# Optimization experiments

Measured on AMD Instinct MI355X. Metric: run time of the kernel, lower is better.

## Reference

```python
import jax, jax.numpy as jnp
import numpy as np

N = 100000      # nodes
E = 1600000     # edges (avg degree 16)
D_IN, D_H, D_OUT = 128, 128, 64


def setup_inputs() -> dict:
    key = jax.random.key(0)
    ks = jax.random.split(key, 9)
    x = jax.random.normal(ks[0], (N, D_IN), dtype=jnp.float32)
    edge_index = jax.random.randint(ks[1], (2, E), 0, N, dtype=jnp.int32)
    edge_weight = jax.random.uniform(ks[2], (E,), dtype=jnp.float32)
    def lin(k, fi, fo):
        return jax.random.normal(k, (fi, fo), dtype=jnp.float32) * np.float32(1.0 / np.sqrt(fi))
    w0 = lin(ks[3], D_IN, D_H);  b0 = jnp.zeros((D_H,), jnp.float32)
    w1 = lin(ks[4], D_H, D_H);   b1 = jnp.zeros((D_H,), jnp.float32)
    w2 = lin(ks[5], D_H, D_OUT); b2 = jnp.zeros((D_OUT,), jnp.float32)
    return {"x": x, "edge_index": edge_index, "edge_weight": edge_weight,
            "w0": w0, "b0": b0, "w1": w1, "b1": b1, "w2": w2, "b2": b2}


def _gcn_conv(x, row, col, norm, w, b):
    # x: [N, fi] -> [N, fo].  PyG GCNConv: linear, gather src, scale, scatter to dst, + bias
    h = x @ w                                   # [N, fo]
    msg = h[row] * norm[:, None]                # [E+N, fo] gather + scale
    out = jax.ops.segment_sum(msg, col, num_segments=N)  # scatter-add to dst
    return out + b


def reference(x, edge_index, edge_weight, w0, b0, w1, b1, w2, b2):
    # add self-loops with weight 1 (PyG gcn_norm default)
    loops = jnp.arange(N, dtype=edge_index.dtype)
    row = jnp.concatenate([edge_index[0], loops])
    col = jnp.concatenate([edge_index[1], loops])
    ew = jnp.concatenate([edge_weight, jnp.ones((N,), edge_weight.dtype)])
    deg = jax.ops.segment_sum(ew, col, num_segments=N)          # in-degree by weight
    dis = jnp.where(deg > 0, jax.lax.rsqrt(deg), 0.0)
    norm = dis[row] * dis[col] * ew                             # [E+N]

    h = _gcn_conv(x, row, col, norm, w0, b0)
    h = jax.nn.relu(h)                                          # dropout: eval mode (identity)
    h = _gcn_conv(h, row, col, norm, w1, b1)
    h = jax.nn.relu(h)
    out = _gcn_conv(h, row, col, norm, w2, b2)
    return out
```

## Files before the change

### kernel.cpp

```cpp
#include <hip/hip_runtime.h>
#include <hip/hip_fp16.h>

typedef __attribute__((ext_vector_type(8))) short bf16x8;
typedef __attribute__((ext_vector_type(4))) float f32x4;

#define EW_SCALE (1.0f / 32767.0f)
#define NBMAX 1024
#define BCAP  4096
#define CHUNK 3072

__device__ __forceinline__ unsigned bf16_rne(float v) {
  unsigned u = __float_as_uint(v);
  return (u + 0x7FFFu + ((u >> 16) & 1u)) >> 16;
}

__global__ __launch_bounds__(256) void bin_fill(const int* __restrict__ row,
    const int* __restrict__ col, const float* __restrict__ ew,
    int* __restrict__ gcnt, uint2* __restrict__ binned, int E) {
  __shared__ uint2 stage[CHUNK];
  __shared__ int cnt_s[NBMAX];
  __shared__ int off_s[NBMAX];
  __shared__ int cur_s[NBMAX];
  __shared__ int gb_s[NBMAX];
  __shared__ int partial[256];
  const int t = threadIdx.x;
  const int base = blockIdx.x * CHUNK;
  const int n = min(CHUNK, E - base);
  for (int k = t; k < NBMAX; k += 256) cnt_s[k] = 0;
  __syncthreads();
  for (int k = t; k < n; k += 256) atomicAdd(&cnt_s[((unsigned)col[base + k]) >> 7], 1);
  __syncthreads();
  int loc[4]; int s0 = 0;
#pragma unroll
  for (int j = 0; j < 4; ++j) { loc[j] = cnt_s[t * 4 + j]; s0 += loc[j]; }
  partial[t] = s0;
  __syncthreads();
  for (int o = 1; o < 256; o <<= 1) {
    int x = (t >= o) ? partial[t - o] : 0;
    __syncthreads();
    partial[t] += x;
    __syncthreads();
  }
  int run = partial[t] - s0;
#pragma unroll
  for (int j = 0; j < 4; ++j) { off_s[t * 4 + j] = run; cur_s[t * 4 + j] = run; run += loc[j]; }
  __syncthreads();
  for (int b = t; b < NBMAX; b += 256) {
    int c = cnt_s[b];
    if (c > 0) gb_s[b] = atomicAdd(&gcnt[b], c);
  }
  for (int k = t; k < n; k += 256) {
    int e = base + k;
    int s = row[e];
    unsigned d = (unsigned)col[e];
    int q = (int)(ew[e] * 32767.0f + 0.5f); if (q > 32767) q = 32767;
    uint2 r = make_uint2(((unsigned)s << 15) | (unsigned)q, d);
    int p = atomicAdd(&cur_s[d >> 7], 1);
    stage[p] = r;
  }
  __syncthreads();
  for (int k = t; k < n; k += 256) {
    uint2 r = stage[k];
    int b = r.y >> 7;
    int pos = gb_s[b] + (k - off_s[b]);
    if (pos < BCAP) binned[(long)b * BCAP + pos] = r;
  }
}

__global__ __launch_bounds__(256) void bucket_build(const uint2* __restrict__ binned,
    const int* __restrict__ gcnt, unsigned* __restrict__ slots,
    int* __restrict__ pdeg, float* __restrict__ dis, int N) {
  __shared__ int cur[128];
  __shared__ float acc[128];
  const int b = blockIdx.x, t = threadIdx.x;
  const int node0 = b << 7;
  int cnt = gcnt[b]; if (cnt > BCAP) cnt = BCAP;
  if (t < 128) { cur[t] = 0; acc[t] = 0.f; }
  __syncthreads();
  for (int k = t; k < cnt; k += 256) {
    uint2 r = binned[(long)b * BCAP + k];
    int nl = r.y & 127;
    int p = atomicAdd(&cur[nl], 1);
    if (p < 64) {
      slots[(long)(node0 + nl) * 64 + p] = r.x;
      atomicAdd(&acc[nl], (float)(r.x & 0x7FFFu) * EW_SCALE);
    }
  }
  __syncthreads();
  if (t < 128) {
    int node = node0 + t;
    if (node < N) {
      int deg = cur[t]; if (deg > 64) deg = 64;
      int pad = (deg + 7) & ~7;
      for (int j = deg; j < pad; ++j) slots[(long)node * 64 + j] = 0u;
      pdeg[node] = pad;
      dis[node] = rsqrtf(1.0f + acc[t]);
    }
  }
}

template<int FO>
__device__ __forceinline__ void prep_w_dev(const float* __restrict__ w,
    ushort* __restrict__ wp, int idx) {
  constexpr int GROUPS = (FO / 16) * 4 * 64;
  constexpr int PLANE  = GROUPS * 8;
  if (idx >= GROUPS) return;
  int l = idx & 63;
  int ts = idx >> 6;
  int s = ts & 3, t = ts >> 2;
  unsigned hi[8], lo[8];
#pragma unroll
  for (int j = 0; j < 8; ++j) {
    float v = w[(s * 32 + (l >> 4) * 8 + j) * FO + t * 16 + (l & 15)];
    unsigned r = bf16_rne(v);
    hi[j] = r;
    float res = v - __uint_as_float(r << 16);
    lo[j] = bf16_rne(res);
  }
  uint4 ph, pl;
  ph.x = hi[0] | (hi[1] << 16); ph.y = hi[2] | (hi[3] << 16);
  ph.z = hi[4] | (hi[5] << 16); ph.w = hi[6] | (hi[7] << 16);
  pl.x = lo[0] | (lo[1] << 16); pl.y = lo[2] | (lo[3] << 16);
  pl.z = lo[4] | (lo[5] << 16); pl.w = lo[6] | (lo[7] << 16);
  *reinterpret_cast<uint4*>(&wp[idx * 8])         = ph;
  *reinterpret_cast<uint4*>(&wp[PLANE + idx * 8]) = pl;
}

__global__ __launch_bounds__(256) void prep_all(const float* __restrict__ w0,
    const float* __restrict__ w1, const float* __restrict__ w2,
    ushort* __restrict__ wp0, ushort* __restrict__ wp1, ushort* __restrict__ wp2,
    int* __restrict__ gcnt) {
  const int b = blockIdx.x, t = threadIdx.x;
  if (b < 8)       prep_w_dev<128>(w0, wp0, b * 256 + t);
  else if (b < 16) prep_w_dev<128>(w1, wp1, (b - 8) * 256 + t);
  else if (b < 20) prep_w_dev<64>(w2, wp2, (b - 16) * 256 + t);
  else { int k = (b - 20) * 256 + t; if (k < NBMAX) gcnt[k] = 0; }
}

template<int FO, bool HIN>
__global__ __launch_bounds__(256) void gemm_mfma(const void* __restrict__ inv,
    const ushort* __restrict__ wp, const float* __restrict__ dis,
    __half* __restrict__ out, int M) {
  constexpr int NT = FO / 16;
  constexpr int PLANE = NT * 4 * 64 * 8;
  __shared__ __attribute__((aligned(16))) ushort sW[2 * PLANE];
  const int tid = threadIdx.x;
  for (int i = tid; i < PLANE / 4; i += 256)
    reinterpret_cast<uint4*>(sW)[i] = reinterpret_cast<const uint4*>(wp)[i];
  __syncthreads();

  const int wave = tid >> 6, lane = tid & 63;
  const int rowA = blockIdx.x * 64 + wave * 16 + (lane & 15);
  const int kblk = lane >> 4;
  const bool rowok = rowA < M;

  f32x4 acc[NT];
#pragma unroll
  for (int t = 0; t < NT; ++t) acc[t] = (f32x4){0.f, 0.f, 0.f, 0.f};

#pragma unroll
  for (int s = 0; s < 4; ++s) {
    float v[8];
    if (rowok) {
      if constexpr (HIN) {
        const __half* inH = (const __half*)inv;
        __half hv[8];
        *reinterpret_cast<uint4*>(hv) =
            *reinterpret_cast<const uint4*>(&inH[(long)rowA * 128 + s * 32 + kblk * 8]);
#pragma unroll
        for (int j = 0; j < 8; ++j) v[j] = __half2float(hv[j]);
      } else {
        const float* inF = (const float*)inv;
        float4 p0 = *reinterpret_cast<const float4*>(&inF[(long)rowA * 128 + s * 32 + kblk * 8]);
        float4 p1 = *reinterpret_cast<const float4*>(&inF[(long)rowA * 128 + s * 32 + kblk * 8 + 4]);
        v[0] = p0.x; v[1] = p0.y; v[2] = p0.z; v[3] = p0.w;
        v[4] = p1.x; v[5] = p1.y; v[6] = p1.z; v[7] = p1.w;
      }
    } else {
#pragma unroll
      for (int j = 0; j < 8; ++j) v[j] = 0.f;
    }
    bf16x8 ah, al;
#pragma unroll
    for (int j = 0; j < 8; ++j) {
      unsigned r = bf16_rne(v[j]);
      ah[j] = (short)(ushort)r;
      float res = v[j] - __uint_as_float(r << 16);
      al[j] = (short)(ushort)bf16_rne(res);
    }
#pragma unroll
    for (int t = 0; t < NT; ++t) {
      bf16x8 bh = *reinterpret_cast<const bf16x8*>(&sW[((t * 4 + s) * 64 + lane) * 8]);
      bf16x8 bl = *reinterpret_cast<const bf16x8*>(&sW[PLANE + ((t * 4 + s) * 64 + lane) * 8]);
      acc[t] = __builtin_amdgcn_mfma_f32_16x16x32_bf16(ah, bh, acc[t], 0, 0, 0);
      acc[t] = __builtin_amdgcn_mfma_f32_16x16x32_bf16(ah, bl, acc[t], 0, 0, 0);
      acc[t] = __builtin_amdgcn_mfma_f32_16x16x32_bf16(al, bh, acc[t], 0, 0, 0);
    }
  }

  const int rbase = blockIdx.x * 64 + wave * 16 + (lane >> 4) * 4;
#pragma unroll
  for (int r = 0; r < 4; ++r) {
    int rr = rbase + r;
    if (rr < M) {
      float ds = dis[rr];
#pragma unroll
      for (int t = 0; t < NT; ++t)
        out[(long)rr * FO + t * 16 + (lane & 15)] = __float2half_rn(ds * acc[t][r]);
    }
  }
}

template<bool RELU>
__global__ __launch_bounds__(256) void agg128_kernel(const __half* __restrict__ g,
    const int* __restrict__ pdeg, const unsigned* __restrict__ slots,
    const float* __restrict__ dis, const float* __restrict__ bias,
    __half* __restrict__ out, int N) {
  const int wave = threadIdx.x >> 6, lane = threadIdx.x & 63;
  const int i = blockIdx.x * 4 + wave;
  if (i >= N) return;
  const int iu = __builtin_amdgcn_readfirstlane(i);
  const __half2* __restrict__ gp = reinterpret_cast<const __half2*>(g);
  const float d = dis[iu];
  const float2 gv = __half22float2(gp[(long)iu * 64 + lane]);
  const int dp = pdeg[iu];
  const unsigned* __restrict__ sp = slots + ((long)iu << 6);
  float accx = 0.f, accy = 0.f;
  for (int j = 0; j < dp; j += 8) {
    uint4 a = *reinterpret_cast<const uint4*>(sp + j);
    uint4 b = *reinterpret_cast<const uint4*>(sp + j + 4);
    __half2 h0 = gp[((long)(a.x >> 15) << 6) + lane];
    __half2 h1 = gp[((long)(a.y >> 15) << 6) + lane];
    __half2 h2 = gp[((long)(a.z >> 15) << 6) + lane];
    __half2 h3 = gp[((long)(a.w >> 15) << 6) + lane];
    __half2 h4 = gp[((long)(b.x >> 15) << 6) + lane];
    __half2 h5 = gp[((long)(b.y >> 15) << 6) + lane];
    __half2 h6 = gp[((long)(b.z >> 15) << 6) + lane];
    __half2 h7 = gp[((long)(b.w >> 15) << 6) + lane];
    float w0 = (float)(a.x & 0x7FFFu), w1 = (float)(a.y & 0x7FFFu);
    float w2 = (float)(a.z & 0x7FFFu), w3 = (float)(a.w & 0x7FFFu);
    float w4 = (float)(b.x & 0x7FFFu), w5 = (float)(b.y & 0x7FFFu);
    float w6 = (float)(b.z & 0x7FFFu), w7 = (float)(b.w & 0x7FFFu);
    accx = fmaf(w0, __low2float(h0), accx); accy = fmaf(w0, __high2float(h0), accy);
    accx = fmaf(w1, __low2float(h1), accx); accy = fmaf(w1, __high2float(h1), accy);
    accx = fmaf(w2, __low2float(h2), accx); accy = fmaf(w2, __high2float(h2), accy);
    accx = fmaf(w3, __low2float(h3), accx); accy = fmaf(w3, __high2float(h3), accy);
    accx = fmaf(w4, __low2float(h4), accx); accy = fmaf(w4, __high2float(h4), accy);
    accx = fmaf(w5, __low2float(h5), accx); accy = fmaf(w5, __high2float(h5), accy);
    accx = fmaf(w6, __low2float(h6), accx); accy = fmaf(w6, __high2float(h6), accy);
    accx = fmaf(w7, __low2float(h7), accx); accy = fmaf(w7, __high2float(h7), accy);
  }
  const float2 bv = reinterpret_cast<const float2*>(bias)[lane];
  float vx = fmaf(d, fmaf(EW_SCALE, accx, gv.x), bv.x);
  float vy = fmaf(d, fmaf(EW_SCALE, accy, gv.y), bv.y);
  if (RELU) { vx = fmaxf(vx, 0.f); vy = fmaxf(vy, 0.f); }
  reinterpret_cast<__half2*>(out)[(long)i * 64 + lane] = __floats2half2_rn(vx, vy);
}

template<bool RELU>
__global__ __launch_bounds__(256) void agg64_kernel(const __half* __restrict__ g,
    const int* __restrict__ pdeg, const unsigned* __restrict__ slots,
    const float* __restrict__ dis, const float* __restrict__ bias,
    float* __restrict__ out, int N) {
  const int wave = threadIdx.x >> 6, lane = threadIdx.x & 63;
  const int i = blockIdx.x * 4 + wave;
  if (i >= N) return;
  const int iu = __builtin_amdgcn_readfirstlane(i);
  const float d = dis[iu];
  const float gv = __half2float(g[(long)iu * 64 + lane]);
  const int dp = pdeg[iu];
  const unsigned* __restrict__ sp = slots + ((long)iu << 6);
  float acc = 0.f;
  for (int j = 0; j < dp; j += 8) {
    uint4 a = *reinterpret_cast<const uint4*>(sp + j);
    uint4 b = *reinterpret_cast<const uint4*>(sp + j + 4);
    __half h0 = g[((long)(a.x >> 15) << 6) + lane];
    __half h1 = g[((long)(a.y >> 15) << 6) + lane];
    __half h2 = g[((long)(a.z >> 15) << 6) + lane];
    __half h3 = g[((long)(a.w >> 15) << 6) + lane];
    __half h4 = g[((long)(b.x >> 15) << 6) + lane];
    __half h5 = g[((long)(b.y >> 15) << 6) + lane];
    __half h6 = g[((long)(b.z >> 15) << 6) + lane];
    __half h7 = g[((long)(b.w >> 15) << 6) + lane];
    acc = fmaf((float)(a.x & 0x7FFFu), __half2float(h0), acc);
    acc = fmaf((float)(a.y & 0x7FFFu), __half2float(h1), acc);
    acc = fmaf((float)(a.z & 0x7FFFu), __half2float(h2), acc);
    acc = fmaf((float)(a.w & 0x7FFFu), __half2float(h3), acc);
    acc = fmaf((float)(b.x & 0x7FFFu), __half2float(h4), acc);
    acc = fmaf((float)(b.y & 0x7FFFu), __half2float(h5), acc);
    acc = fmaf((float)(b.z & 0x7FFFu), __half2float(h6), acc);
    acc = fmaf((float)(b.w & 0x7FFFu), __half2float(h7), acc);
  }
  float v = fmaf(d, fmaf(EW_SCALE, acc, gv), bias[lane]);
  if (RELU) v = fmaxf(v, 0.f);
  out[(long)i * 64 + lane] = v;
}

extern "C" void kernel_launch(void* const* d_in, const int* in_sizes, int n_in,
                              void* d_out, int out_size, void* d_ws, size_t ws_size,
                              hipStream_t stream) {
  const float* x  = (const float*)d_in[0];
  const int*   ei = (const int*)  d_in[1];
  const float* ew = (const float*)d_in[2];
  const float* w0 = (const float*)d_in[3];
  const float* b0 = (const float*)d_in[4];
  const float* w1 = (const float*)d_in[5];
  const float* b1 = (const float*)d_in[6];
  const float* w2 = (const float*)d_in[7];
  const float* b2 = (const float*)d_in[8];

  const int N = in_sizes[0] / 128;
  const int E = in_sizes[2];
  const int* row = ei;
  const int* col = ei + E;
  const int NB = (N + 127) / 128;

  auto align16 = [](size_t v) { return (v + 15) & ~(size_t)15; };
  const long NF = (long)N * 128;

  size_t off = 0;
  __half*   bufA   = (__half*)((char*)d_ws + off); off = align16(off + NF * sizeof(__half));
  __half*   bufB   = (__half*)((char*)d_ws + off); off = align16(off + NF * sizeof(__half));
  unsigned* slots  = (unsigned*)((char*)d_ws + off); off = align16(off + (size_t)N * 64 * 4);
  uint2*    binned = (uint2*)((char*)d_ws + off); off = align16(off + (size_t)NB * BCAP * 8);
  int*      gcnt   = (int*)((char*)d_ws + off); off = align16(off + (size_t)NBMAX * 4);
  int*      pdeg   = (int*)((char*)d_ws + off); off = align16(off + (size_t)N * 4);
  float*    dis    = (float*)((char*)d_ws + off); off = align16(off + (size_t)N * 4);
  const size_t WP128 = 2ull * 8 * 4 * 64 * 8 * sizeof(ushort);
  ushort*   wp0    = (ushort*)((char*)d_ws + off); off += WP128;
  ushort*   wp1    = (ushort*)((char*)d_ws + off); off += WP128;
  ushort*   wp2    = (ushort*)((char*)d_ws + off); off += WP128 / 2;
  if (ws_size < off) return;

  auto cdiv = [](long a, long b) { return (int)((a + b - 1) / b); };

  prep_all<<<24, 256, 0, stream>>>(w0, w1, w2, wp0, wp1, wp2, gcnt);

  bin_fill    <<<cdiv(E,CHUNK),256,0,stream>>>(row, col, ew, gcnt, binned, E);
  bucket_build<<<NB,256,0,stream>>>(binned, gcnt, slots, pdeg, dis, N);

  gemm_mfma<128,false><<<cdiv(N,64),256,0,stream>>>(x, wp0, dis, bufA, N);
  agg128_kernel<true><<<cdiv(N,4),256,0,stream>>>(bufA, pdeg, slots, dis, b0, bufB, N);
  gemm_mfma<128,true><<<cdiv(N,64),256,0,stream>>>(bufB, wp1, dis, bufA, N);
  agg128_kernel<true><<<cdiv(N,4),256,0,stream>>>(bufA, pdeg, slots, dis, b1, bufB, N);
  gemm_mfma<64,true><<<cdiv(N,64),256,0,stream>>>(bufB, wp2, dis, bufA, N);
  agg64_kernel<false><<<cdiv(N,4),256,0,stream>>>(bufA, pdeg, slots, dis, b2, (float*)d_out, N);
}
```

Measured before the change: 277.9 us.

## Fuse aggregation with next-layer GEMM via LDS-staged bf16 split tiles

Merges each 128-wide aggregation (bias, ReLU) with the following layer's MFMA GEMM. Each block aggregates 64 nodes into XOR-swizzled LDS as hi/lo bf16 pairs, then multiplies them by the weights, which are read straight from global memory. This removes the fp16 round trip of the intermediate activations and two launches. The first GEMM now processes 128 rows per block so its weight staging is amortised. The risk is lower occupancy, since each wave serially gathers 16 nodes before the MFMA phase, with no overlap between gather and compute.

```diff
diff --git a/kernel.cpp b/kernel.cpp
--- a/kernel.cpp
+++ b/kernel.cpp
@@ -137,11 +137,10 @@
   else { int k = (b - 20) * 256 + t; if (k < NBMAX) gcnt[k] = 0; }
 }
 
-template<int FO, bool HIN>
-__global__ __launch_bounds__(256) void gemm_mfma(const void* __restrict__ inv,
+__global__ __launch_bounds__(256) void gemm0(const float* __restrict__ in,
     const ushort* __restrict__ wp, const float* __restrict__ dis,
     __half* __restrict__ out, int M) {
-  constexpr int NT = FO / 16;
+  constexpr int NT = 8;
   constexpr int PLANE = NT * 4 * 64 * 8;
   __shared__ __attribute__((aligned(16))) ushort sW[2 * PLANE];
   const int tid = threadIdx.x;
@@ -150,114 +149,153 @@
   __syncthreads();
 
   const int wave = tid >> 6, lane = tid & 63;
-  const int rowA = blockIdx.x * 64 + wave * 16 + (lane & 15);
   const int kblk = lane >> 4;
-  const bool rowok = rowA < M;
-
-  f32x4 acc[NT];
-#pragma unroll
-  for (int t = 0; t < NT; ++t) acc[t] = (f32x4){0.f, 0.f, 0.f, 0.f};
-
-#pragma unroll
-  for (int s = 0; s < 4; ++s) {
-    float v[8];
-    if (rowok) {
-      if constexpr (HIN) {
-        const __half* inH = (const __half*)inv;
-        __half hv[8];
-        *reinterpret_cast<uint4*>(hv) =
-            *reinterpret_cast<const uint4*>(&inH[(long)rowA * 128 + s * 32 + kblk * 8]);
-#pragma unroll
-        for (int j = 0; j < 8; ++j) v[j] = __half2float(hv[j]);
-      } else {
-        const float* inF = (const float*)inv;
-        float4 p0 = *reinterpret_cast<const float4*>(&inF[(long)rowA * 128 + s * 32 + kblk * 8]);
-        float4 p1 = *reinterpret_cast<const float4*>(&inF[(long)rowA * 128 + s * 32 + kblk * 8 + 4]);
+
+  for (int half = 0; half < 2; ++half) {
+    const int rowA = blockIdx.x * 128 + half * 64 + wave * 16 + (lane & 15);
+    const bool rowok = rowA < M;
+    f32x4 acc[NT];
+#pragma unroll
+    for (int t = 0; t < NT; ++t) acc[t] = (f32x4){0.f, 0.f, 0.f, 0.f};
+#pragma unroll
+    for (int s = 0; s < 4; ++s) {
+      float v[8];
+      if (rowok) {
+        float4 p0 = *reinterpret_cast<const float4*>(&in[(long)rowA * 128 + s * 32 + kblk * 8]);
+        float4 p1 = *reinterpret_cast<const float4*>(&in[(long)rowA * 128 + s * 32 + kblk * 8 + 4]);
         v[0] = p0.x; v[1] = p0.y; v[2] = p0.z; v[3] = p0.w;
         v[4] = p1.x; v[5] = p1.y; v[6] = p1.z; v[7] = p1.w;
-      }
-    } else {
-#pragma unroll
-      for (int j = 0; j < 8; ++j) v[j] = 0.f;
-    }
-    bf16x8 ah, al;
-#pragma unroll
-    for (int j = 0; j < 8; ++j) {
-      unsigned r = bf16_rne(v[j]);
-      ah[j] = (short)(ushort)r;
-      float res = v[j] - __uint_as_float(r << 16);
-      al[j] = (short)(ushort)bf16_rne(res);
-    }
+      } else {
+#pragma unroll
+        for (int j = 0; j < 8; ++j) v[j] = 0.f;
+      }
+      bf16x8 ah, al;
+#pragma unroll
+      for (int j = 0; j < 8; ++j) {
+        unsigned r = bf16_rne(v[j]);
+        ah[j] = (short)(ushort)r;
+        float res = v[j] - __uint_as_float(r << 16);
+        al[j] = (short)(ushort)bf16_rne(res);
+      }
+#pragma unroll
+      for (int t = 0; t < NT; ++t) {
+        bf16x8 bh = *reinterpret_cast<const bf16x8*>(&sW[((t * 4 + s) * 64 + lane) * 8]);
+        bf16x8 bl = *reinterpret_cast<const bf16x8*>(&sW[PLANE + ((t * 4 + s) * 64 + lane) * 8]);
+        acc[t] = __builtin_amdgcn_mfma_f32_16x16x32_bf16(ah, bh, acc[t], 0, 0, 0);
+        acc[t] = __builtin_amdgcn_mfma_f32_16x16x32_bf16(ah, bl, acc[t], 0, 0, 0);
+        acc[t] = __builtin_amdgcn_mfma_f32_16x16x32_bf16(al, bh, acc[t], 0, 0, 0);
+      }
+    }
+    const int rbase = blockIdx.x * 128 + half * 64 + wave * 16 + (lane >> 4) * 4;
+#pragma unroll
+    for (int r = 0; r < 4; ++r) {
+      int rr = rbase + r;
+      if (rr < M) {
+        float ds = dis[rr];
+#pragma unroll
+        for (int t = 0; t < NT; ++t)
+          out[(long)rr * 128 + t * 16 + (lane & 15)] = __float2half_rn(ds * acc[t][r]);
+      }
+    }
+  }
+}
+
+template<int FO>
+__global__ __launch_bounds__(256) void fused_agg_gemm(const __half* __restrict__ g,
+    const int* __restrict__ pdeg, const unsigned* __restrict__ slots,
+    const float* __restrict__ dis, const float* __restrict__ bias,
+    const ushort* __restrict__ wp, __half* __restrict__ out, int N) {
+  constexpr int NT = FO / 16;
+  constexpr int PLANE = NT * 4 * 64 * 8;
+  __shared__ __attribute__((aligned(16))) unsigned tHi[64 * 64];
+  __shared__ __attribute__((aligned(16))) unsigned tLo[64 * 64];
+  const int tid = threadIdx.x;
+  const int w = tid >> 6, lane = tid & 63;
+  const int base = blockIdx.x * 64;
+  const __half2* __restrict__ gp = reinterpret_cast<const __half2*>(g);
+  const float2 bv = reinterpret_cast<const float2*>(bias)[lane];
+
+  for (int k = 0; k < 16; ++k) {
+    const int r = w * 16 + k;
+    const int node = __builtin_amdgcn_readfirstlane(base + r);
+    float vx = 0.f, vy = 0.f;
+    if (node < N) {
+      const float d = dis[node];
+      const float2 gv = __half22float2(gp[(long)node * 64 + lane]);
+      const int dp = pdeg[node];
+      const unsigned* __restrict__ sp = slots + ((long)node << 6);
+      float accx = 0.f, accy = 0.f;
+      for (int j = 0; j < dp; j += 8) {
+        uint4 a = *reinterpret_cast<const uint4*>(sp + j);
+        uint4 b = *reinterpret_cast<const uint4*>(sp + j + 4);
+        __half2 h0 = gp[((long)(a.x >> 15) << 6) + lane];
+        __half2 h1 = gp[((long)(a.y >> 15) << 6) + lane];
+        __half2 h2 = gp[((long)(a.z >> 15) << 6) + lane];
+        __half2 h3 = gp[((long)(a.w >> 15) << 6) + lane];
+        __half2 h4 = gp[((long)(b.x >> 15) << 6) + lane];
+        __half2 h5 = gp[((long)(b.y >> 15) << 6) + lane];
+        __half2 h6 = gp[((long)(b.z >> 15) << 6) + lane];
+        __half2 h7 = gp[((long)(b.w >> 15) << 6) + lane];
+        float w0 = (float)(a.x & 0x7FFFu), w1 = (float)(a.y & 0x7FFFu);
+        float w2 = (float)(a.z & 0x7FFFu), w3 = (float)(a.w & 0x7FFFu);
+        float w4 = (float)(b.x & 0x7FFFu), w5 = (float)(b.y & 0x7FFFu);
+        float w6 = (float)(b.z & 0x7FFFu), w7 = (float)(b.w & 0x7FFFu);
+        accx = fmaf(w0, __low2float(h0), accx); accy = fmaf(w0, __high2float(h0), accy);
+        accx = fmaf(w1, __low2float(h1), accx); accy = fmaf(w1, __high2float(h1), accy);
+        accx = fmaf(w2, __low2float(h2), accx); accy = fmaf(w2, __high2float(h2), accy);
+        accx = fmaf(w3, __low2float(h3), accx); accy = fmaf(w3, __high2float(h3), accy);
+        accx = fmaf(w4, __low2float(h4), accx); accy = fmaf(w4, __high2float(h4), accy);
+        accx = fmaf(w5, __low2float(h5), accx); accy = fmaf(w5, __high2float(h5), accy);
+        accx = fmaf(w6, __low2float(h6), accx); accy = fmaf(w6, __high2float(h6), accy);
+        accx = fmaf(w7, __low2float(h7), accx); accy = fmaf(w7, __high2float(h7), accy);
+      }
+      vx = fmaxf(fmaf(d, fmaf(EW_SCALE, accx, gv.x), bv.x), 0.f);
+      vy = fmaxf(fmaf(d, fmaf(EW_SCALE, accy, gv.y), bv.y), 0.f);
+    }
+    unsigned hx = bf16_rne(vx), hy = bf16_rne(vy);
+    float rx = vx - __uint_as_float(hx << 16);
+    float ry = vy - __uint_as_float(hy << 16);
+    unsigned lx = bf16_rne(rx), ly = bf16_rne(ry);
+    const int phys = (lane >> 2) ^ k;
+    const int idx = r * 64 + phys * 4 + (lane & 3);
+    tHi[idx] = hx | (hy << 16);
+    tLo[idx] = lx | (ly << 16);
+  }
+  __syncthreads();
+
+  const int r15 = lane & 15, kblk = lane >> 4;
+  f32x4 acc[NT];
+#pragma unroll
+  for (int t = 0; t < NT; ++t) acc[t] = (f32x4){0.f, 0.f, 0.f, 0.f};
+#pragma unroll
+  for (int s = 0; s < 4; ++s) {
+    const int slot = s * 4 + kblk;
+    const int phys = slot ^ r15;
+    const int idx = (w * 16 + r15) * 64 + phys * 4;
+    bf16x8 ah = *reinterpret_cast<const bf16x8*>(&tHi[idx]);
+    bf16x8 al = *reinterpret_cast<const bf16x8*>(&tLo[idx]);
 #pragma unroll
     for (int t = 0; t < NT; ++t) {
-      bf16x8 bh = *reinterpret_cast<const bf16x8*>(&sW[((t * 4 + s) * 64 + lane) * 8]);
-      bf16x8 bl = *reinterpret_cast<const bf16x8*>(&sW[PLANE + ((t * 4 + s) * 64 + lane) * 8]);
+      bf16x8 bh = *reinterpret_cast<const bf16x8*>(&wp[((t * 4 + s) * 64 + lane) * 8]);
+      bf16x8 bl = *reinterpret_cast<const bf16x8*>(&wp[PLANE + ((t * 4 + s) * 64 + lane) * 8]);
       acc[t] = __builtin_amdgcn_mfma_f32_16x16x32_bf16(ah, bh, acc[t], 0, 0, 0);
       acc[t] = __builtin_amdgcn_mfma_f32_16x16x32_bf16(ah, bl, acc[t], 0, 0, 0);
       acc[t] = __builtin_amdgcn_mfma_f32_16x16x32_bf16(al, bh, acc[t], 0, 0, 0);
     }
   }
-
-  const int rbase = blockIdx.x * 64 + wave * 16 + (lane >> 4) * 4;
+  const int rbase = base + w * 16 + (lane >> 4) * 4;
 #pragma unroll
   for (int r = 0; r < 4; ++r) {
     int rr = rbase + r;
-    if (rr < M) {
+    if (rr < N) {
       float ds = dis[rr];
 #pragma unroll
       for (int t = 0; t < NT; ++t)
-        out[(long)rr * FO + t * 16 + (lane & 15)] = __float2half_rn(ds * acc[t][r]);
-    }
-  }
-}
-
-template<bool RELU>
-__global__ __launch_bounds__(256) void agg128_kernel(const __half* __restrict__ g,
-    const int* __restrict__ pdeg, const unsigned* __restrict__ slots,
-    const float* __restrict__ dis, const float* __restrict__ bias,
-    __half* __restrict__ out, int N) {
-  const int wave = threadIdx.x >> 6, lane = threadIdx.x & 63;
-  const int i = blockIdx.x * 4 + wave;
-  if (i >= N) return;
-  const int iu = __builtin_amdgcn_readfirstlane(i);
-  const __half2* __restrict__ gp = reinterpret_cast<const __half2*>(g);
-  const float d = dis[iu];
-  const float2 gv = __half22float2(gp[(long)iu * 64 + lane]);
-  const int dp = pdeg[iu];
-  const unsigned* __restrict__ sp = slots + ((long)iu << 6);
-  float accx = 0.f, accy = 0.f;
-  for (int j = 0; j < dp; j += 8) {
-    uint4 a = *reinterpret_cast<const uint4*>(sp + j);
-    uint4 b = *reinterpret_cast<const uint4*>(sp + j + 4);
-    __half2 h0 = gp[((long)(a.x >> 15) << 6) + lane];
-    __half2 h1 = gp[((long)(a.y >> 15) << 6) + lane];
-    __half2 h2 = gp[((long)(a.z >> 15) << 6) + lane];
-    __half2 h3 = gp[((long)(a.w >> 15) << 6) + lane];
-    __half2 h4 = gp[((long)(b.x >> 15) << 6) + lane];
-    __half2 h5 = gp[((long)(b.y >> 15) << 6) + lane];
-    __half2 h6 = gp[((long)(b.z >> 15) << 6) + lane];
-    __half2 h7 = gp[((long)(b.w >> 15) << 6) + lane];
-    float w0 = (float)(a.x & 0x7FFFu), w1 = (float)(a.y & 0x7FFFu);
-    float w2 = (float)(a.z & 0x7FFFu), w3 = (float)(a.w & 0x7FFFu);
-    float w4 = (float)(b.x & 0x7FFFu), w5 = (float)(b.y & 0x7FFFu);
-    float w6 = (float)(b.z & 0x7FFFu), w7 = (float)(b.w & 0x7FFFu);
-    accx = fmaf(w0, __low2float(h0), accx); accy = fmaf(w0, __high2float(h0), accy);
-    accx = fmaf(w1, __low2float(h1), accx); accy = fmaf(w1, __high2float(h1), accy);
-    accx = fmaf(w2, __low2float(h2), accx); accy = fmaf(w2, __high2float(h2), accy);
-    accx = fmaf(w3, __low2float(h3), accx); accy = fmaf(w3, __high2float(h3), accy);
-    accx = fmaf(w4, __low2float(h4), accx); accy = fmaf(w4, __high2float(h4), accy);
-    accx = fmaf(w5, __low2float(h5), accx); accy = fmaf(w5, __high2float(h5), accy);
-    accx = fmaf(w6, __low2float(h6), accx); accy = fmaf(w6, __high2float(h6), accy);
-    accx = fmaf(w7, __low2float(h7), accx); accy = fmaf(w7, __high2float(h7), accy);
-  }
-  const float2 bv = reinterpret_cast<const float2*>(bias)[lane];
-  float vx = fmaf(d, fmaf(EW_SCALE, accx, gv.x), bv.x);
-  float vy = fmaf(d, fmaf(EW_SCALE, accy, gv.y), bv.y);
-  if (RELU) { vx = fmaxf(vx, 0.f); vy = fmaxf(vy, 0.f); }
-  reinterpret_cast<__half2*>(out)[(long)i * 64 + lane] = __floats2half2_rn(vx, vy);
-}
-
-template<bool RELU>
+        out[(long)rr * FO + t * 16 + r15] = __float2half_rn(ds * acc[t][r]);
+    }
+  }
+}
+
 __global__ __launch_bounds__(256) void agg64_kernel(const __half* __restrict__ g,
     const int* __restrict__ pdeg, const unsigned* __restrict__ slots,
     const float* __restrict__ dis, const float* __restrict__ bias,
@@ -292,7 +330,6 @@
     acc = fmaf((float)(b.w & 0x7FFFu), __half2float(h7), acc);
   }
   float v = fmaf(d, fmaf(EW_SCALE, acc, gv), bias[lane]);
-  if (RELU) v = fmaxf(v, 0.f);
   out[(long)i * 64 + lane] = v;
 }
 
@@ -339,10 +376,8 @@
   bin_fill    <<<cdiv(E,CHUNK),256,0,stream>>>(row, col, ew, gcnt, binned, E);
   bucket_build<<<NB,256,0,stream>>>(binned, gcnt, slots, pdeg, dis, N);
 
-  gemm_mfma<128,false><<<cdiv(N,64),256,0,stream>>>(x, wp0, dis, bufA, N);
-  agg128_kernel<true><<<cdiv(N,4),256,0,stream>>>(bufA, pdeg, slots, dis, b0, bufB, N);
-  gemm_mfma<128,true><<<cdiv(N,64),256,0,stream>>>(bufB, wp1, dis, bufA, N);
-  agg128_kernel<true><<<cdiv(N,4),256,0,stream>>>(bufA, pdeg, slots, dis, b1, bufB, N);
-  gemm_mfma<64,true><<<cdiv(N,64),256,0,stream>>>(bufB, wp2, dis, bufA, N);
-  agg64_kernel<false><<<cdiv(N,4),256,0,stream>>>(bufA, pdeg, slots, dis, b2, (float*)d_out, N);
-}
+  gemm0<<<cdiv(N,128),256,0,stream>>>(x, wp0, dis, bufA, N);
+  fused_agg_gemm<128><<<cdiv(N,64),256,0,stream>>>(bufA, pdeg, slots, dis, b0, wp1, bufB, N);
+  fused_agg_gemm<64><<<cdiv(N,64),256,0,stream>>>(bufB, pdeg, slots, dis, b1, wp2, bufA, N);
+  agg64_kernel<<<cdiv(N,4),256,0,stream>>>(bufA, pdeg, slots, dis, b2, (float*)d_out, N);
+}
```

New measurement: 279.6 us. Within noise of the previous version (+0.6%).

## Fuse edge binning with first GEMM and move source normalization into aggregation

Applied to the files above, without the earlier changes.

The first-layer GEMM no longer depends on the degree normalization, because the source-side dis scaling now happens inside the aggregation kernels as a per-edge dis[src] gather. That lets the binning, the layer-0 GEMM with in-block weight prep, and the w1/w2 prep run in one combined launch instead of several serial ones. The GEMMs now handle 128 rows per block, and the gcnt reset becomes a memset. The cost is an extra random dis gather per edge in every aggregation pass, plus a combined kernel whose 64KB shared allocation applies to every block.

```diff
diff --git a/kernel.cpp b/kernel.cpp
--- a/kernel.cpp
+++ b/kernel.cpp
@@ -12,91 +12,6 @@
 __device__ __forceinline__ unsigned bf16_rne(float v) {
   unsigned u = __float_as_uint(v);
   return (u + 0x7FFFu + ((u >> 16) & 1u)) >> 16;
-}
-
-__global__ __launch_bounds__(256) void bin_fill(const int* __restrict__ row,
-    const int* __restrict__ col, const float* __restrict__ ew,
-    int* __restrict__ gcnt, uint2* __restrict__ binned, int E) {
-  __shared__ uint2 stage[CHUNK];
-  __shared__ int cnt_s[NBMAX];
-  __shared__ int off_s[NBMAX];
-  __shared__ int cur_s[NBMAX];
-  __shared__ int gb_s[NBMAX];
-  __shared__ int partial[256];
-  const int t = threadIdx.x;
-  const int base = blockIdx.x * CHUNK;
-  const int n = min(CHUNK, E - base);
-  for (int k = t; k < NBMAX; k += 256) cnt_s[k] = 0;
-  __syncthreads();
-  for (int k = t; k < n; k += 256) atomicAdd(&cnt_s[((unsigned)col[base + k]) >> 7], 1);
-  __syncthreads();
-  int loc[4]; int s0 = 0;
-#pragma unroll
-  for (int j = 0; j < 4; ++j) { loc[j] = cnt_s[t * 4 + j]; s0 += loc[j]; }
-  partial[t] = s0;
-  __syncthreads();
-  for (int o = 1; o < 256; o <<= 1) {
-    int x = (t >= o) ? partial[t - o] : 0;
-    __syncthreads();
-    partial[t] += x;
-    __syncthreads();
-  }
-  int run = partial[t] - s0;
-#pragma unroll
-  for (int j = 0; j < 4; ++j) { off_s[t * 4 + j] = run; cur_s[t * 4 + j] = run; run += loc[j]; }
-  __syncthreads();
-  for (int b = t; b < NBMAX; b += 256) {
-    int c = cnt_s[b];
-    if (c > 0) gb_s[b] = atomicAdd(&gcnt[b], c);
-  }
-  for (int k = t; k < n; k += 256) {
-    int e = base + k;
-    int s = row[e];
-    unsigned d = (unsigned)col[e];
-    int q = (int)(ew[e] * 32767.0f + 0.5f); if (q > 32767) q = 32767;
-    uint2 r = make_uint2(((unsigned)s << 15) | (unsigned)q, d);
-    int p = atomicAdd(&cur_s[d >> 7], 1);
-    stage[p] = r;
-  }
-  __syncthreads();
-  for (int k = t; k < n; k += 256) {
-    uint2 r = stage[k];
-    int b = r.y >> 7;
-    int pos = gb_s[b] + (k - off_s[b]);
-    if (pos < BCAP) binned[(long)b * BCAP + pos] = r;
-  }
-}
-
-__global__ __launch_bounds__(256) void bucket_build(const uint2* __restrict__ binned,
-    const int* __restrict__ gcnt, unsigned* __restrict__ slots,
-    int* __restrict__ pdeg, float* __restrict__ dis, int N) {
-  __shared__ int cur[128];
-  __shared__ float acc[128];
-  const int b = blockIdx.x, t = threadIdx.x;
-  const int node0 = b << 7;
-  int cnt = gcnt[b]; if (cnt > BCAP) cnt = BCAP;
-  if (t < 128) { cur[t] = 0; acc[t] = 0.f; }
-  __syncthreads();
-  for (int k = t; k < cnt; k += 256) {
-    uint2 r = binned[(long)b * BCAP + k];
-    int nl = r.y & 127;
-    int p = atomicAdd(&cur[nl], 1);
-    if (p < 64) {
-      slots[(long)(node0 + nl) * 64 + p] = r.x;
-      atomicAdd(&acc[nl], (float)(r.x & 0x7FFFu) * EW_SCALE);
-    }
-  }
-  __syncthreads();
-  if (t < 128) {
-    int node = node0 + t;
-    if (node < N) {
-      int deg = cur[t]; if (deg > 64) deg = 64;
-      int pad = (deg + 7) & ~7;
-      for (int j = deg; j < pad; ++j) slots[(long)node * 64 + j] = 0u;
-      pdeg[node] = pad;
-      dis[node] = rsqrtf(1.0f + acc[t]);
-    }
-  }
 }
 
 template<int FO>
@@ -126,21 +41,183 @@
   *reinterpret_cast<uint4*>(&wp[PLANE + idx * 8]) = pl;
 }
 
-__global__ __launch_bounds__(256) void prep_all(const float* __restrict__ w0,
-    const float* __restrict__ w1, const float* __restrict__ w2,
-    ushort* __restrict__ wp0, ushort* __restrict__ wp1, ushort* __restrict__ wp2,
-    int* __restrict__ gcnt) {
+__device__ void bin_fill_dev(const int* __restrict__ row, const int* __restrict__ col,
+    const float* __restrict__ ew, int* __restrict__ gcnt, uint2* __restrict__ binned,
+    int E, int blk, int t, char* smem) {
+  uint2* stage = (uint2*)smem;
+  int* cnt_s = (int*)(smem + 24576);
+  int* off_s = cnt_s + NBMAX;
+  int* cur_s = off_s + NBMAX;
+  int* gb_s  = cur_s + NBMAX;
+  int* partial = gb_s + NBMAX;
+  const int base = blk * CHUNK;
+  const int n = min(CHUNK, E - base);
+  for (int k = t; k < NBMAX; k += 256) cnt_s[k] = 0;
+  __syncthreads();
+  for (int k = t; k < n; k += 256) atomicAdd(&cnt_s[((unsigned)col[base + k]) >> 7], 1);
+  __syncthreads();
+  int loc[4]; int s0 = 0;
+#pragma unroll
+  for (int j = 0; j < 4; ++j) { loc[j] = cnt_s[t * 4 + j]; s0 += loc[j]; }
+  partial[t] = s0;
+  __syncthreads();
+  for (int o = 1; o < 256; o <<= 1) {
+    int x = (t >= o) ? partial[t - o] : 0;
+    __syncthreads();
+    partial[t] += x;
+    __syncthreads();
+  }
+  int run = partial[t] - s0;
+#pragma unroll
+  for (int j = 0; j < 4; ++j) { off_s[t * 4 + j] = run; cur_s[t * 4 + j] = run; run += loc[j]; }
+  __syncthreads();
+  for (int b = t; b < NBMAX; b += 256) {
+    int c = cnt_s[b];
+    if (c > 0) gb_s[b] = atomicAdd(&gcnt[b], c);
+  }
+  for (int k = t; k < n; k += 256) {
+    int e = base + k;
+    int s = row[e];
+    unsigned d = (unsigned)col[e];
+    int q = (int)(ew[e] * 32767.0f + 0.5f); if (q > 32767) q = 32767;
+    uint2 r = make_uint2(((unsigned)s << 15) | (unsigned)q, d);
+    int p = atomicAdd(&cur_s[d >> 7], 1);
+    stage[p] = r;
+  }
+  __syncthreads();
+  for (int k = t; k < n; k += 256) {
+    uint2 r = stage[k];
+    int b = r.y >> 7;
+    int pos = gb_s[b] + (k - off_s[b]);
+    if (pos < BCAP) binned[(long)b * BCAP + pos] = r;
+  }
+}
+
+__device__ void gemm0_dev(const float* __restrict__ in, const float* __restrict__ w0,
+    __half* __restrict__ out, int M, int blk, int tid, ushort* sW) {
+  constexpr int NT = 8;
+  constexpr int PLANE = NT * 4 * 64 * 8;
+  for (int idx = tid; idx < NT * 4 * 64; idx += 256) {
+    int l = idx & 63, ts = idx >> 6, s = ts & 3, tt = ts >> 2;
+    unsigned hi[8], lo[8];
+#pragma unroll
+    for (int j = 0; j < 8; ++j) {
+      float v = w0[(s * 32 + (l >> 4) * 8 + j) * 128 + tt * 16 + (l & 15)];
+      unsigned r = bf16_rne(v);
+      hi[j] = r;
+      float res = v - __uint_as_float(r << 16);
+      lo[j] = bf16_rne(res);
+    }
+    uint4 ph, pl;
+    ph.x = hi[0] | (hi[1] << 16); ph.y = hi[2] | (hi[3] << 16);
+    ph.z = hi[4] | (hi[5] << 16); ph.w = hi[6] | (hi[7] << 16);
+    pl.x = lo[0] | (lo[1] << 16); pl.y = lo[2] | (lo[3] << 16);
+    pl.z = lo[4] | (lo[5] << 16); pl.w = lo[6] | (lo[7] << 16);
+    *reinterpret_cast<uint4*>(&sW[idx * 8])         = ph;
+    *reinterpret_cast<uint4*>(&sW[PLANE + idx * 8]) = pl;
+  }
+  __syncthreads();
+
+  const int wave = tid >> 6, lane = tid & 63;
+  const int kblk = lane >> 4, r15 = lane & 15;
+  for (int half = 0; half < 2; ++half) {
+    const int rowA = blk * 128 + half * 64 + wave * 16 + r15;
+    const bool rowok = rowA < M;
+    f32x4 acc[NT];
+#pragma unroll
+    for (int t = 0; t < NT; ++t) acc[t] = (f32x4){0.f, 0.f, 0.f, 0.f};
+#pragma unroll
+    for (int s = 0; s < 4; ++s) {
+      float v[8];
+      if (rowok) {
+        float4 p0 = *reinterpret_cast<const float4*>(&in[(long)rowA * 128 + s * 32 + kblk * 8]);
+        float4 p1 = *reinterpret_cast<const float4*>(&in[(long)rowA * 128 + s * 32 + kblk * 8 + 4]);
+        v[0] = p0.x; v[1] = p0.y; v[2] = p0.z; v[3] = p0.w;
+        v[4] = p1.x; v[5] = p1.y; v[6] = p1.z; v[7] = p1.w;
+      } else {
+#pragma unroll
+        for (int j = 0; j < 8; ++j) v[j] = 0.f;
+      }
+      bf16x8 ah, al;
+#pragma unroll
+      for (int j = 0; j < 8; ++j) {
+        unsigned r = bf16_rne(v[j]);
+        ah[j] = (short)(ushort)r;
+        float res = v[j] - __uint_as_float(r << 16);
+        al[j] = (short)(ushort)bf16_rne(res);
+      }
+#pragma unroll
+      for (int t = 0; t < NT; ++t) {
+        bf16x8 bh = *reinterpret_cast<const bf16x8*>(&sW[((t * 4 + s) * 64 + lane) * 8]);
+        bf16x8 bl = *reinterpret_cast<const bf16x8*>(&sW[PLANE + ((t * 4 + s) * 64 + lane) * 8]);
+        acc[t] = __builtin_amdgcn_mfma_f32_16x16x32_bf16(ah, bh, acc[t], 0, 0, 0);
+        acc[t] = __builtin_amdgcn_mfma_f32_16x16x32_bf16(ah, bl, acc[t], 0, 0, 0);
+        acc[t] = __builtin_amdgcn_mfma_f32_16x16x32_bf16(al, bh, acc[t], 0, 0, 0);
+      }
+    }
+    const int rbase = blk * 128 + half * 64 + wave * 16 + (lane >> 4) * 4;
+#pragma unroll
+    for (int r = 0; r < 4; ++r) {
+      int rr = rbase + r;
+      if (rr < M) {
+#pragma unroll
+        for (int t = 0; t < NT; ++t)
+          out[(long)rr * 128 + t * 16 + r15] = __float2half_rn(acc[t][r]);
+      }
+    }
+  }
+}
+
+__global__ __launch_bounds__(256) void combo0(const float* __restrict__ x,
+    const float* __restrict__ w0, const float* __restrict__ w1, const float* __restrict__ w2,
+    ushort* __restrict__ wp1, ushort* __restrict__ wp2,
+    const int* __restrict__ row, const int* __restrict__ col, const float* __restrict__ ew,
+    int* __restrict__ gcnt, uint2* __restrict__ binned, __half* __restrict__ bufA,
+    int N, int E, int NBF, int G0) {
+  __shared__ __attribute__((aligned(16))) char smem[65536];
+  const int b = blockIdx.x, tid = threadIdx.x;
+  if (b < NBF) { bin_fill_dev(row, col, ew, gcnt, binned, E, b, tid, smem); return; }
+  if (b < NBF + G0) { gemm0_dev(x, w0, bufA, N, b - NBF, tid, (ushort*)smem); return; }
+  int pb = b - NBF - G0;
+  if (pb < 8) prep_w_dev<128>(w1, wp1, pb * 256 + tid);
+  else        prep_w_dev<64>(w2, wp2, (pb - 8) * 256 + tid);
+}
+
+__global__ __launch_bounds__(256) void bucket_build(const uint2* __restrict__ binned,
+    const int* __restrict__ gcnt, unsigned* __restrict__ slots,
+    int* __restrict__ pdeg, float* __restrict__ dis, int N) {
+  __shared__ int cur[128];
+  __shared__ float acc[128];
   const int b = blockIdx.x, t = threadIdx.x;
-  if (b < 8)       prep_w_dev<128>(w0, wp0, b * 256 + t);
-  else if (b < 16) prep_w_dev<128>(w1, wp1, (b - 8) * 256 + t);
-  else if (b < 20) prep_w_dev<64>(w2, wp2, (b - 16) * 256 + t);
-  else { int k = (b - 20) * 256 + t; if (k < NBMAX) gcnt[k] = 0; }
-}
-
-template<int FO, bool HIN>
-__global__ __launch_bounds__(256) void gemm_mfma(const void* __restrict__ inv,
-    const ushort* __restrict__ wp, const float* __restrict__ dis,
-    __half* __restrict__ out, int M) {
+  const int node0 = b << 7;
+  int cnt = gcnt[b]; if (cnt > BCAP) cnt = BCAP;
+  if (t < 128) { cur[t] = 0; acc[t] = 0.f; }
+  __syncthreads();
+  for (int k = t; k < cnt; k += 256) {
+    uint2 r = binned[(long)b * BCAP + k];
+    int nl = r.y & 127;
+    int p = atomicAdd(&cur[nl], 1);
+    if (p < 64) {
+      slots[(long)(node0 + nl) * 64 + p] = r.x;
+      atomicAdd(&acc[nl], (float)(r.x & 0x7FFFu) * EW_SCALE);
+    }
+  }
+  __syncthreads();
+  if (t < 128) {
+    int node = node0 + t;
+    if (node < N) {
+      int deg = cur[t]; if (deg > 64) deg = 64;
+      int pad = (deg + 7) & ~7;
+      for (int j = deg; j < pad; ++j) slots[(long)node * 64 + j] = 0u;
+      pdeg[node] = pad;
+      dis[node] = rsqrtf(1.0f + acc[t]);
+    }
+  }
+}
+
+template<int FO>
+__global__ __launch_bounds__(256) void gemm_mfma(const __half* __restrict__ in,
+    const ushort* __restrict__ wp, __half* __restrict__ out, int M) {
   constexpr int NT = FO / 16;
   constexpr int PLANE = NT * 4 * 64 * 8;
   __shared__ __attribute__((aligned(16))) ushort sW[2 * PLANE];
@@ -150,63 +227,52 @@
   __syncthreads();
 
   const int wave = tid >> 6, lane = tid & 63;
-  const int rowA = blockIdx.x * 64 + wave * 16 + (lane & 15);
-  const int kblk = lane >> 4;
-  const bool rowok = rowA < M;
-
-  f32x4 acc[NT];
-#pragma unroll
-  for (int t = 0; t < NT; ++t) acc[t] = (f32x4){0.f, 0.f, 0.f, 0.f};
-
-#pragma unroll
-  for (int s = 0; s < 4; ++s) {
-    float v[8];
-    if (rowok) {
-      if constexpr (HIN) {
-        const __half* inH = (const __half*)inv;
+  const int kblk = lane >> 4, r15 = lane & 15;
+  for (int half = 0; half < 2; ++half) {
+    const int rowA = blockIdx.x * 128 + half * 64 + wave * 16 + r15;
+    const bool rowok = rowA < M;
+    f32x4 acc[NT];
+#pragma unroll
+    for (int t = 0; t < NT; ++t) acc[t] = (f32x4){0.f, 0.f, 0.f, 0.f};
+#pragma unroll
+    for (int s = 0; s < 4; ++s) {
+      float v[8];
+      if (rowok) {
         __half hv[8];
         *reinterpret_cast<uint4*>(hv) =
-            *reinterpret_cast<const uint4*>(&inH[(long)rowA * 128 + s * 32 + kblk * 8]);
+            *reinterpret_cast<const uint4*>(&in[(long)rowA * 128 + s * 32 + kblk * 8]);
 #pragma unroll
         for (int j = 0; j < 8; ++j) v[j] = __half2float(hv[j]);
       } else {
-        const float* inF = (const float*)inv;
-        float4 p0 = *reinterpret_cast<const float4*>(&inF[(long)rowA * 128 + s * 32 + kblk * 8]);
-        float4 p1 = *reinterpret_cast<const float4*>(&inF[(long)rowA * 128 + s * 32 + kblk * 8 + 4]);
-        v[0] = p0.x; v[1] = p0.y; v[2] = p0.z; v[3] = p0.w;
-        v[4] = p1.x; v[5] = p1.y; v[6] = p1.z; v[7] = p1.w;
-      }
-    } else {
-#pragma unroll
-      for (int j = 0; j < 8; ++j) v[j] = 0.f;
-    }
-    bf16x8 ah, al;
-#pragma unroll
-    for (int j = 0; j < 8; ++j) {
-      unsigned r = bf16_rne(v[j]);
-      ah[j] = (short)(ushort)r;
-      float res = v[j] - __uint_as_float(r << 16);
-      al[j] = (short)(ushort)bf16_rne(res);
-    }
-#pragma unroll
-    for (int t = 0; t < NT; ++t) {
-      bf16x8 bh = *reinterpret_cast<const bf16x8*>(&sW[((t * 4 + s) * 64 + lane) * 8]);
-      bf16x8 bl = *reinterpret_cast<const bf16x8*>(&sW[PLANE + ((t * 4 + s) * 64 + lane) * 8]);
-      acc[t] = __builtin_amdgcn_mfma_f32_16x16x32_bf16(ah, bh, acc[t], 0, 0, 0);
-      acc[t] = __builtin_amdgcn_mfma_f32_16x16x32_bf16(ah, bl, acc[t], 0, 0, 0);
-      acc[t] = __builtin_amdgcn_mfma_f32_16x16x32_bf16(al, bh, acc[t], 0, 0, 0);
-    }
-  }
-
-  const int rbase = blockIdx.x * 64 + wave * 16 + (lane >> 4) * 4;
-#pragma unroll
-  for (int r = 0; r < 4; ++r) {
-    int rr = rbase + r;
-    if (rr < M) {
-      float ds = dis[rr];
-#pragma unroll
-      for (int t = 0; t < NT; ++t)
-        out[(long)rr * FO + t * 16 + (lane & 15)] = __float2half_rn(ds * acc[t][r]);
+#pragma unroll
+        for (int j = 0; j < 8; ++j) v[j] = 0.f;
+      }
+      bf16x8 ah, al;
+#pragma unroll
+      for (int j = 0; j < 8; ++j) {
+        unsigned r = bf16_rne(v[j]);
+        ah[j] = (short)(ushort)r;
+        float res = v[j] - __uint_as_float(r << 16);
+        al[j] = (short)(ushort)bf16_rne(res);
+      }
+#pragma unroll
+      for (int t = 0; t < NT; ++t) {
+        bf16x8 bh = *reinterpret_cast<const bf16x8*>(&sW[((t * 4 + s) * 64 + lane) * 8]);
+        bf16x8 bl = *reinterpret_cast<const bf16x8*>(&sW[PLANE + ((t * 4 + s) * 64 + lane) * 8]);
+        acc[t] = __builtin_amdgcn_mfma_f32_16x16x32_bf16(ah, bh, acc[t], 0, 0, 0);
+        acc[t] = __builtin_amdgcn_mfma_f32_16x16x32_bf16(ah, bl, acc[t], 0, 0, 0);
+        acc[t] = __builtin_amdgcn_mfma_f32_16x16x32_bf16(al, bh, acc[t], 0, 0, 0);
+      }
+    }
+    const int rbase = blockIdx.x * 128 + half * 64 + wave * 16 + (lane >> 4) * 4;
+#pragma unroll
+    for (int r = 0; r < 4; ++r) {
+      int rr = rbase + r;
+      if (rr < M) {
+#pragma unroll
+        for (int t = 0; t < NT; ++t)
+          out[(long)rr * FO + t * 16 + r15] = __float2half_rn(acc[t][r]);
+      }
     }
   }
 }
@@ -221,7 +287,7 @@
   if (i >= N) return;
   const int iu = __builtin_amdgcn_readfirstlane(i);
   const __half2* __restrict__ gp = reinterpret_cast<const __half2*>(g);
-  const float d = dis[iu];
+  const float dd = dis[iu];
   const float2 gv = __half22float2(gp[(long)iu * 64 + lane]);
   const int dp = pdeg[iu];
   const unsigned* __restrict__ sp = slots + ((long)iu << 6);
@@ -237,10 +303,14 @@
     __half2 h5 = gp[((long)(b.y >> 15) << 6) + lane];
     __half2 h6 = gp[((long)(b.z >> 15) << 6) + lane];
     __half2 h7 = gp[((long)(b.w >> 15) << 6) + lane];
-    float w0 = (float)(a.x & 0x7FFFu), w1 = (float)(a.y & 0x7FFFu);
-    float w2 = (float)(a.z & 0x7FFFu), w3 = (float)(a.w & 0x7FFFu);
-    float w4 = (float)(b.x & 0x7FFFu), w5 = (float)(b.y & 0x7FFFu);
-    float w6 = (float)(b.z & 0x7FFFu), w7 = (float)(b.w & 0x7FFFu);
+    float w0 = (float)(a.x & 0x7FFFu) * dis[a.x >> 15];
+    float w1 = (float)(a.y & 0x7FFFu) * dis[a.y >> 15];
+    float w2 = (float)(a.z & 0x7FFFu) * dis[a.z >> 15];
+    float w3 = (float)(a.w & 0x7FFFu) * dis[a.w >> 15];
+    float w4 = (float)(b.x & 0x7FFFu) * dis[b.x >> 15];
+    float w5 = (float)(b.y & 0x7FFFu) * dis[b.y >> 15];
+    float w6 = (float)(b.z & 0x7FFFu) * dis[b.z >> 15];
+    float w7 = (float)(b.w & 0x7FFFu) * dis[b.w >> 15];
     accx = fmaf(w0, __low2float(h0), accx); accy = fmaf(w0, __high2float(h0), accy);
     accx = fmaf(w1, __low2float(h1), accx); accy = fmaf(w1, __high2float(h1), accy);
     accx = fmaf(w2, __low2float(h2), accx); accy = fmaf(w2, __high2float(h2), accy);
@@ -251,13 +321,13 @@
     accx = fmaf(w7, __low2float(h7), accx); accy = fmaf(w7, __high2float(h7), accy);
   }
   const float2 bv = reinterpret_cast<const float2*>(bias)[lane];
-  float vx = fmaf(d, fmaf(EW_SCALE, accx, gv.x), bv.x);
-  float vy = fmaf(d, fmaf(EW_SCALE, accy, gv.y), bv.y);
+  const float dds = dd * EW_SCALE, dd2 = dd * dd;
+  float vx = fmaf(dds, accx, fmaf(dd2, gv.x, bv.x));
+  float vy = fmaf(dds, accy, fmaf(dd2, gv.y, bv.y));
   if (RELU) { vx = fmaxf(vx, 0.f); vy = fmaxf(vy, 0.f); }
   reinterpret_cast<__half2*>(out)[(long)i * 64 + lane] = __floats2half2_rn(vx, vy);
 }
 
-template<bool RELU>
 __global__ __launch_bounds__(256) void agg64_kernel(const __half* __restrict__ g,
     const int* __restrict__ pdeg, const unsigned* __restrict__ slots,
     const float* __restrict__ dis, const float* __restrict__ bias,
@@ -266,7 +336,7 @@
   const int i = blockIdx.x * 4 + wave;
   if (i >= N) return;
   const int iu = __builtin_amdgcn_readfirstlane(i);
-  const float d = dis[iu];
+  const float dd = dis[iu];
   const float gv = __half2float(g[(long)iu * 64 + lane]);
   const int dp = pdeg[iu];
   const unsigned* __restrict__ sp = slots + ((long)iu << 6);
@@ -282,18 +352,25 @@
     __half h5 = g[((long)(b.y >> 15) << 6) + lane];
     __half h6 = g[((long)(b.z >> 15) << 6) + lane];
     __half h7 = g[((long)(b.w >> 15) << 6) + lane];
-    acc = fmaf((float)(a.x & 0x7FFFu), __half2float(h0), acc);
-    acc = fmaf((float)(a.y & 0x7FFFu), __half2float(h1), acc);
-    acc = fmaf((float)(a.z & 0x7FFFu), __half2float(h2), acc);
-    acc = fmaf((float)(a.w & 0x7FFFu), __half2float(h3), acc);
-    acc = fmaf((float)(b.x & 0x7FFFu), __half2float(h4), acc);
-    acc = fmaf((float)(b.y & 0x7FFFu), __half2float(h5), acc);
-    acc = fmaf((float)(b.z & 0x7FFFu), __half2float(h6), acc);
-    acc = fmaf((float)(b.w & 0x7FFFu), __half2float(h7), acc);
-  }
-  float v = fmaf(d, fmaf(EW_SCALE, acc, gv), bias[lane]);
-  if (RELU) v = fmaxf(v, 0.f);
-  out[(long)i * 64 + lane] = v;
+    float w0 = (float)(a.x & 0x7FFFu) * dis[a.x >> 15];
+    float w1 = (float)(a.y & 0x7FFFu) * dis[a.y >> 15];
+    float w2 = (float)(a.z & 0x7FFFu) * dis[a.z >> 15];
+    float w3 = (float)(a.w & 0x7FFFu) * dis[a.w >> 15];
+    float w4 = (float)(b.x & 0x7FFFu) * dis[b.x >> 15];
+    float w5 = (float)(b.y & 0x7FFFu) * dis[b.y >> 15];
+    float w6 = (float)(b.z & 0x7FFFu) * dis[b.z >> 15];
+    float w7 = (float)(b.w & 0x7FFFu) * dis[b.w >> 15];
+    acc = fmaf(w0, __half2float(h0), acc);
+    acc = fmaf(w1, __half2float(h1), acc);
+    acc = fmaf(w2, __half2float(h2), acc);
+    acc = fmaf(w3, __half2float(h3), acc);
+    acc = fmaf(w4, __half2float(h4), acc);
+    acc = fmaf(w5, __half2float(h5), acc);
+    acc = fmaf(w6, __half2float(h6), acc);
+    acc = fmaf(w7, __half2float(h7), acc);
+  }
+  const float dds = dd * EW_SCALE, dd2 = dd * dd;
+  out[(long)i * 64 + lane] = fmaf(dds, acc, fmaf(dd2, gv, bias[lane]));
 }
 
 extern "C" void kernel_launch(void* const* d_in, const int* in_sizes, int n_in,
@@ -327,22 +404,22 @@
   int*      pdeg   = (int*)((char*)d_ws + off); off = align16(off + (size_t)N * 4);
   float*    dis    = (float*)((char*)d_ws + off); off = align16(off + (size_t)N * 4);
   const size_t WP128 = 2ull * 8 * 4 * 64 * 8 * sizeof(ushort);
-  ushort*   wp0    = (ushort*)((char*)d_ws + off); off += WP128;
   ushort*   wp1    = (ushort*)((char*)d_ws + off); off += WP128;
   ushort*   wp2    = (ushort*)((char*)d_ws + off); off += WP128 / 2;
   if (ws_size < off) return;
 
   auto cdiv = [](long a, long b) { return (int)((a + b - 1) / b); };
-
-  prep_all<<<24, 256, 0, stream>>>(w0, w1, w2, wp0, wp1, wp2, gcnt);
-
-  bin_fill    <<<cdiv(E,CHUNK),256,0,stream>>>(row, col, ew, gcnt, binned, E);
+  const int NBF = cdiv(E, CHUNK);
+  const int G0  = cdiv(N, 128);
+
+  hipMemsetAsync(gcnt, 0, (size_t)NBMAX * sizeof(int), stream);
+  combo0<<<NBF + G0 + 12, 256, 0, stream>>>(x, w0, w1, w2, wp1, wp2,
+                                            row, col, ew, gcnt, binned, bufA, N, E, NBF, G0);
   bucket_build<<<NB,256,0,stream>>>(binned, gcnt, slots, pdeg, dis, N);
 
-  gemm_mfma<128,false><<<cdiv(N,64),256,0,stream>>>(x, wp0, dis, bufA, N);
   agg128_kernel<true><<<cdiv(N,4),256,0,stream>>>(bufA, pdeg, slots, dis, b0, bufB, N);
-  gemm_mfma<128,true><<<cdiv(N,64),256,0,stream>>>(bufB, wp1, dis, bufA, N);
+  gemm_mfma<128><<<cdiv(N,128),256,0,stream>>>(bufB, wp1, bufA, N);
   agg128_kernel<true><<<cdiv(N,4),256,0,stream>>>(bufA, pdeg, slots, dis, b1, bufB, N);
-  gemm_mfma<64,true><<<cdiv(N,64),256,0,stream>>>(bufB, wp2, dis, bufA, N);
-  agg64_kernel<false><<<cdiv(N,4),256,0,stream>>>(bufA, pdeg, slots, dis, b2, (float*)d_out, N);
-}
+  gemm_mfma<64><<<cdiv(N,128),256,0,stream>>>(bufB, wp2, bufA, N);
+  agg64_kernel<<<cdiv(N,4),256,0,stream>>>(bufA, pdeg, slots, dis, b2, (float*)d_out, N);
+}
```

New measurement: 294.2 us. +5.9%, slower.
